# Kernel optimization log

Hardware: AMD Instinct MI355X
Metric: run time of the kernel (lower is better)

The kernel has to match this reference:

```python
import jax, jax.numpy as jnp
import numpy as np

D_VOC, P_VOC, M_VOC = 2048, 1024, 4096
H = 256
T = 32
LD, LP, LM = 24, 12, 20


def _norm_adj(key, n):
    # binary graph + self loops, row-normalized (matches GCN.normalize(adj+I))
    a = (jax.random.uniform(key, (n, n)) < 0.002).astype(jnp.float32)
    a = a + jnp.eye(n, dtype=jnp.float32)
    rs = a.sum(axis=1)
    rinv = jnp.where(rs > 0, 1.0 / rs, 0.0)
    return rinv[:, None] * a


def setup_inputs() -> dict:
    key = jax.random.key(0)
    ks = jax.random.split(key, 32)
    s = float(1.0 / np.sqrt(H))
    u = lambda k, shape, sc: jax.random.uniform(k, shape, minval=-sc, maxval=sc, dtype=jnp.float32)
    inp = {
        'diag_codes': jax.random.randint(ks[0], (T, LD), 0, D_VOC),
        'proc_codes': jax.random.randint(ks[1], (T, LP), 0, P_VOC),
        'med_codes': jax.random.randint(ks[2], (T - 1, LM), 0, M_VOC),
        'diag_emb': u(ks[3], (D_VOC, H), 0.1),
        'proc_emb': u(ks[4], (P_VOC, H), 0.1),
        'gru_d_wih': u(ks[5], (3 * H, H), s), 'gru_d_whh': u(ks[6], (3 * H, H), s),
        'gru_d_bih': u(ks[7], (3 * H,), s), 'gru_d_bhh': u(ks[8], (3 * H,), s),
        'gru_p_wih': u(ks[9], (3 * H, H), s), 'gru_p_whh': u(ks[10], (3 * H, H), s),
        'gru_p_bih': u(ks[11], (3 * H,), s), 'gru_p_bhh': u(ks[12], (3 * H,), s),
        'q_w': u(ks[13], (2 * H, H), s), 'q_b': u(ks[14], (H,), s),
        'adj_ehr': _norm_adj(ks[15], M_VOC),
        'adj_ddi': _norm_adj(ks[16], M_VOC),
        'w1_ehr': u(ks[17], (M_VOC, H), s), 'b1_ehr': u(ks[18], (H,), s),
        'w2_ehr': u(ks[19], (H, H), s), 'b2_ehr': u(ks[20], (H,), s),
        'w1_ddi': u(ks[21], (M_VOC, H), s), 'b1_ddi': u(ks[22], (H,), s),
        'w2_ddi': u(ks[23], (H, H), s), 'b2_ddi': u(ks[24], (H,), s),
        'inter': jax.random.normal(ks[25], (1,), dtype=jnp.float32) / H,
        'proj_w': u(ks[26], (2 * H, H), s), 'proj_b': u(ks[27], (H,), s),
    }
    return inp


def _gru(x, wih, whh, bih, bhh):
    # torch.nn.GRU cell math; x: [T, H] -> outputs [T, H]
    def step(h, xt):
        gi = xt @ wih.T + bih
        gh = h @ whh.T + bhh
        ir, iz, inn = jnp.split(gi, 3)
        hr, hz, hn = jnp.split(gh, 3)
        r = jax.nn.sigmoid(ir + hr)
        z = jax.nn.sigmoid(iz + hz)
        n = jnp.tanh(inn + r * hn)
        h2 = (1.0 - z) * n + z * h
        return h2, h2
    _, ys = jax.lax.scan(step, jnp.zeros((x.shape[-1],), x.dtype), x)
    return ys


def _gcn(adj, w1, b1, w2, b2):
    # input features are identity, so first support mm(I, w1) == w1
    h1 = jax.nn.relu(adj @ w1 + b1)
    return adj @ (h1 @ w2) + b2


def reference(diag_codes, proc_codes, med_codes, diag_emb, proc_emb,
              gru_d_wih, gru_d_whh, gru_d_bih, gru_d_bhh,
              gru_p_wih, gru_p_whh, gru_p_bih, gru_p_bhh,
              q_w, q_b, adj_ehr, adj_ddi,
              w1_ehr, b1_ehr, w2_ehr, b2_ehr,
              w1_ddi, b1_ddi, w2_ddi, b2_ddi,
              inter, proj_w, proj_b):
    # ---- PatientEncoder: gather + sum codes per visit, GRU over visits ----
    seq_d = diag_emb[diag_codes].sum(axis=1)            # [T, H]
    seq_p = proc_emb[proc_codes].sum(axis=1)            # [T, H]
    od = _gru(seq_d, gru_d_wih, gru_d_whh, gru_d_bih, gru_d_bhh)
    op = _gru(seq_p, gru_p_wih, gru_p_whh, gru_p_bih, gru_p_bhh)
    feats = jnp.concatenate([od, op], axis=-1)          # [T, 2H]
    queries = jax.nn.relu(feats) @ q_w + q_b            # [T, H] (Sequential(ReLU, Linear))
    query = queries[-1:]                                # [1, H]
    history_keys = queries[:-1]                         # [T-1, H]
    # multi-hot history medication values (scatter)
    tm1 = med_codes.shape[0]
    history_values = jnp.zeros((tm1, M_VOC), jnp.float32).at[
        jnp.arange(tm1)[:, None], med_codes].set(1.0)   # [T-1, M_VOC]
    # ---- PriorEncoder ----
    prior = _gcn(adj_ehr, w1_ehr, b1_ehr, w2_ehr, b2_ehr) \
        - inter[0] * _gcn(adj_ddi, w1_ddi, b1_ddi, w2_ddi, b2_ddi)  # [M_VOC, H]
    w_emb = jax.nn.softmax(query @ prior.T, axis=-1)    # [1, M_VOC]
    # diag(w) @ prior == broadcast row-scale (the fused gather-weighted-scale)
    gc1 = w_emb.reshape(-1, 1) * prior                  # [M_VOC, H]
    visit_w = jax.nn.softmax(query @ history_keys.T, axis=-1)  # [1, T-1]
    wv = (visit_w @ history_values).reshape(-1, 1)      # [M_VOC, 1]
    gc2 = wv * prior                                    # [M_VOC, H]
    return jnp.concatenate([gc1, gc2], axis=-1) @ proj_w + proj_b  # [M_VOC, H]
```

## Files before the change

kernel.cpp:

```cpp
#include <hip/hip_runtime.h>
#include <hip/hip_bf16.h>

#define HD   256
#define TT   32
#define MV   4096
#define LD_  24
#define LP_  12
#define LM_  20
#define MAXNZ 96

typedef _Float16 h2v __attribute__((ext_vector_type(2)));
typedef _Float16 h8  __attribute__((ext_vector_type(8)));

__device__ __forceinline__ float fdot2(h2v a, h2v b, float c) {
#if __has_builtin(__builtin_amdgcn_fdot2)
  return __builtin_amdgcn_fdot2(a, b, c, false);
#else
  return c + (float)a[0] * (float)b[0] + (float)a[1] * (float)b[1];
#endif
}

#define PIN2(x) { float _t = __builtin_bit_cast(float, x); \
                  asm volatile("" : "+v"(_t));             \
                  x = __builtin_bit_cast(h2v, _t); }

__global__ __launch_bounds__(768) void k01_prep(
    const float* __restrict__ whh_d, const float* __restrict__ whh_p,
    h8* __restrict__ wt,
    const int* __restrict__ dc, const int* __restrict__ pc,
    const float* __restrict__ demb, const float* __restrict__ pemb,
    const float* __restrict__ wih_d, const float* __restrict__ bih_d,
    const float* __restrict__ wih_p, const float* __restrict__ bih_p,
    float* __restrict__ GI)
{
  if (blockIdx.y < 2) {
    const int i = blockIdx.x, b = blockIdx.y, g = threadIdx.x;
    const float* whh = b ? whh_p : whh_d;
    const float* src = whh + (size_t)g * HD + 8 * i;
    h8 v;
#pragma unroll
    for (int e = 0; e < 8; ++e) v[e] = (_Float16)src[e];
    wt[((size_t)b * 32 + i) * 768 + g] = v;
    return;
  }
  const int t = blockIdx.x, b = blockIdx.y - 2;
  const int* codes = b ? pc : dc;
  const int L = b ? LP_ : LD_;
  const float* emb = b ? pemb : demb;
  const float* wih = b ? wih_p : wih_d;
  const float* bih = b ? bih_p : bih_d;
  __shared__ float s[HD];
  const int j = threadIdx.x;
  if (j < HD) {
    float acc = 0.f;
    for (int l = 0; l < L; ++l) acc += emb[(size_t)codes[t * L + l] * HD + j];
    s[j] = acc;
  }
  __syncthreads();
  const int g = j;
  float acc = bih[g];
  const float* wr = wih + (size_t)g * HD;
  for (int k = 0; k < HD; k += 4) {
    float4 w4 = *(const float4*)(wr + k);
    acc = fmaf(w4.x, s[k], acc);
    acc = fmaf(w4.y, s[k + 1], acc);
    acc = fmaf(w4.z, s[k + 2], acc);
    acc = fmaf(w4.w, s[k + 3], acc);
  }
  GI[((size_t)b * TT + t) * 768 + g] = acc;
}

#define LOADROW(EV, ADJROW)                                        \
  _Pragma("unroll")                                                \
  for (int c = 0; c < 16; ++c)                                     \
    EV[c] = *(const float4*)((ADJROW) + c * 256 + lane * 4);

#define PROCESS(EV, RG)                                                 \
  {                                                                     \
    int cl = 0;                                                         \
    _Pragma("unroll")                                                   \
    for (int c = 0; c < 16; ++c)                                        \
      cl += (EV[c].x != 0.f) + (EV[c].y != 0.f) +                       \
            (EV[c].z != 0.f) + (EV[c].w != 0.f);                        \
    int pref = cl;                                                      \
    _Pragma("unroll")                                                   \
    for (int ofs = 1; ofs < 64; ofs <<= 1) {                            \
      int v = __shfl_up(pref, ofs, 64);                                 \
      if (lane >= ofs) pref += v;                                       \
    }                                                                   \
    const int total = __shfl(pref, 63, 64);                             \
    int pos = pref - cl;                                                \
    int* cg = cols_g + (size_t)(RG) * MAXNZ;                            \
    float* vg = vals_g + (size_t)(RG) * MAXNZ;                          \
    _Pragma("unroll")                                                   \
    for (int c = 0; c < 16; ++c) {                                      \
      const float vv[4] = {EV[c].x, EV[c].y, EV[c].z, EV[c].w};         \
      _Pragma("unroll")                                                 \
      for (int e = 0; e < 4; ++e) {                                     \
        if (vv[e] != 0.f) {                                             \
          if (pos < MAXNZ) { cg[pos] = c * 256 + lane * 4 + e;          \
                             vg[pos] = vv[e]; }                         \
          ++pos;                                                        \
        }                                                               \
      }                                                                 \
    }                                                                   \
    if (lane == 0) cnt_g[RG] = total > MAXNZ ? MAXNZ : total;           \
  }

#define ROWPTR(RG) (((RG) >> 12 ? adj_d : adj_e) + (size_t)((RG) & (MV - 1)) * MV)

__global__ __launch_bounds__(512)
__attribute__((amdgpu_waves_per_eu(2, 2)))
void k23_fused(
    const float* __restrict__ GI, const h8* __restrict__ wt,
    const float* __restrict__ bhh_d, const float* __restrict__ bhh_p,
    float* __restrict__ feats,
    const float* __restrict__ adj_e, const float* __restrict__ adj_d,
    int* __restrict__ cnt_g, int* __restrict__ cols_g,
    float* __restrict__ vals_g)
{
  __shared__ h8 hbuf[2][32];

  if (blockIdx.x < 2) {
    const int b = blockIdx.x, t = threadIdx.x;
    const int p = t >> 1;
    const int hk = t & 1;
    const float* gi = GI + (size_t)b * TT * 768;
    const float* bhh = b ? bhh_p : bhh_d;

    h2v w[192];
    {
      const h8* wbase = wt + (size_t)b * 32 * 768;
#pragma unroll
      for (int r3 = 0; r3 < 3; ++r3) {
#pragma unroll
        for (int ii = 0; ii < 16; ++ii) {
          union { h8 v; h2v q[4]; } u;
          u.v = wbase[(size_t)(hk * 16 + ii) * 768 + r3 * 256 + p];
          w[(r3 * 16 + ii) * 4 + 0] = u.q[0];
          w[(r3 * 16 + ii) * 4 + 1] = u.q[1];
          w[(r3 * 16 + ii) * 4 + 2] = u.q[2];
          w[(r3 * 16 + ii) * 4 + 3] = u.q[3];
        }
      }
    }
#pragma unroll
    for (int i = 0; i < 192; ++i) PIN2(w[i])

    const float bh_r = bhh[p], bh_z = bhh[256 + p], bh_n = bhh[512 + p];
    float hreg = 0.f;
    if (t < 256) ((_Float16*)&hbuf[0][0])[t] = (_Float16)0.f;
    __syncthreads();

    for (int tt = 0; tt < TT; ++tt) {
      const float* git = gi + tt * 768;
      float ir = 0.f, iz = 0.f, inn = 0.f;
      if (hk == 0) { ir = git[p]; iz = git[256 + p]; inn = git[512 + p]; }

      const h8* hb = hbuf[tt & 1];
      float dr0 = 0.f, dr1 = 0.f, dz0 = 0.f, dz1 = 0.f, dn0 = 0.f, dn1 = 0.f;
#pragma unroll
      for (int ii = 0; ii < 16; ++ii) {
        union { h8 v; h2v q[4]; } u;
        u.v = hb[hk * 16 + ii];
        dr0 = fdot2(w[(0 * 16 + ii) * 4 + 0], u.q[0], dr0);
        dr1 = fdot2(w[(0 * 16 + ii) * 4 + 1], u.q[1], dr1);
        dr0 = fdot2(w[(0 * 16 + ii) * 4 + 2], u.q[2], dr0);
        dr1 = fdot2(w[(0 * 16 + ii) * 4 + 3], u.q[3], dr1);
        dz0 = fdot2(w[(1 * 16 + ii) * 4 + 0], u.q[0], dz0);
        dz1 = fdot2(w[(1 * 16 + ii) * 4 + 1], u.q[1], dz1);
        dz0 = fdot2(w[(1 * 16 + ii) * 4 + 2], u.q[2], dz0);
        dz1 = fdot2(w[(1 * 16 + ii) * 4 + 3], u.q[3], dz1);
        dn0 = fdot2(w[(2 * 16 + ii) * 4 + 0], u.q[0], dn0);
        dn1 = fdot2(w[(2 * 16 + ii) * 4 + 1], u.q[1], dn1);
        dn0 = fdot2(w[(2 * 16 + ii) * 4 + 2], u.q[2], dn0);
        dn1 = fdot2(w[(2 * 16 + ii) * 4 + 3], u.q[3], dn1);
      }
      float dr = dr0 + dr1, dz = dz0 + dz1, dn = dn0 + dn1;
      dr += __shfl_xor(dr, 1, 64);
      dz += __shfl_xor(dz, 1, 64);
      dn += __shfl_xor(dn, 1, 64);
      if (hk == 0) {
        const float hr = dr + bh_r, hz = dz + bh_z, hn = dn + bh_n;
        const float r = 1.f / (1.f + __expf(-(ir + hr)));
        const float z = 1.f / (1.f + __expf(-(iz + hz)));
        const float n = tanhf(inn + r * hn);
        hreg = (1.f - z) * n + z * hreg;
        ((_Float16*)&hbuf[(tt & 1) ^ 1][0])[p] = (_Float16)hreg;
        feats[(size_t)tt * 512 + b * HD + p] = hreg;
      }
      __syncthreads();
    }
    return;
  }

  const int w = threadIdx.x >> 6, lane = threadIdx.x & 63;
  const int rg0 = (blockIdx.x - 2) * 8 + w;
  const int r0 = rg0, r1 = rg0 + 2032, r2 = rg0 + 4064, r3 = rg0 + 6096,
            r4 = rg0 + 8128;
  const bool has5 = (r4 < 2 * MV);

  float4 evA[16], evB[16];
  LOADROW(evA, ROWPTR(r0))
  LOADROW(evB, ROWPTR(r1))
  PROCESS(evA, r0)
  LOADROW(evA, ROWPTR(r2))
  PROCESS(evB, r1)
  LOADROW(evB, ROWPTR(r3))
  PROCESS(evA, r2)
  if (has5) { LOADROW(evA, ROWPTR(r4)) }
  PROCESS(evB, r3)
  if (has5) { PROCESS(evA, r4) }
}

__global__ __launch_bounds__(256) void k2b_queries(
    const float* __restrict__ feats, const float* __restrict__ q_w,
    const float* __restrict__ q_b, float* __restrict__ queries)
{
  const int t = blockIdx.x, j = threadIdx.x;
  __shared__ float f[512];
  f[j] = fmaxf(feats[(size_t)t * 512 + j], 0.f);
  f[j + 256] = fmaxf(feats[(size_t)t * 512 + 256 + j], 0.f);
  __syncthreads();
  float acc = q_b[j];
  for (int k = 0; k < 512; ++k) acc = fmaf(f[k], q_w[(size_t)k * HD + j], acc);
  queries[(size_t)t * HD + j] = acc;
}

__global__ __launch_bounds__(512) void k45_z(
    const int* __restrict__ cnt_g, const int* __restrict__ cols_g,
    const float* __restrict__ vals_g,
    const float* __restrict__ w1_e, const float* __restrict__ b1_e,
    const float* __restrict__ w1_d, const float* __restrict__ b1_d,
    const float* __restrict__ w2_e, const float* __restrict__ w2_d,
    float* __restrict__ zz)
{
  const int blk = blockIdx.x, b = blockIdx.y;
  const int t = threadIdx.x;
  __shared__ float tile[8][HD];
  __shared__ float part[8][HD];

  {
    const int w = t >> 6, lane = t & 63;
    const int rg = b * MV + blk * 8 + w;
    const float* w1 = b ? w1_d : w1_e;
    const float* b1 = b ? b1_d : b1_e;
    const int n = cnt_g[rg];
    const int* cg = cols_g + (size_t)rg * MAXNZ;
    const float* vg = vals_g + (size_t)rg * MAXNZ;
    float4 acc = *(const float4*)(b1 + lane * 4);
    for (int k = 0; k < n; ++k) {
      const int col = cg[k];
      const float v = vg[k];
      const float4 wv4 = *(const float4*)(w1 + (size_t)col * HD + lane * 4);
      acc.x = fmaf(v, wv4.x, acc.x);
      acc.y = fmaf(v, wv4.y, acc.y);
      acc.z = fmaf(v, wv4.z, acc.z);
      acc.w = fmaf(v, wv4.w, acc.w);
    }
    float4* dst = (float4*)&tile[w][lane * 4];
    dst->x = fmaxf(acc.x, 0.f); dst->y = fmaxf(acc.y, 0.f);
    dst->z = fmaxf(acc.z, 0.f); dst->w = fmaxf(acc.w, 0.f);
  }
  __syncthreads();

  const int j = t & 255, half = t >> 8;
  const float* w2 = b ? w2_d : w2_e;
  float acc[8];
#pragma unroll
  for (int r = 0; r < 8; ++r) acc[r] = 0.f;
  const int k0 = half * 128;
  for (int k = k0; k < k0 + 128; k += 4) {
    float wa = w2[(size_t)(k + 0) * HD + j];
    float wb = w2[(size_t)(k + 1) * HD + j];
    float wc = w2[(size_t)(k + 2) * HD + j];
    float wd = w2[(size_t)(k + 3) * HD + j];
#pragma unroll
    for (int r = 0; r < 8; ++r) {
      float4 tv = *(const float4*)&tile[r][k];
      acc[r] = fmaf(tv.x, wa, acc[r]);
      acc[r] = fmaf(tv.y, wb, acc[r]);
      acc[r] = fmaf(tv.z, wc, acc[r]);
      acc[r] = fmaf(tv.w, wd, acc[r]);
    }
  }
  if (half == 1) {
#pragma unroll
    for (int r = 0; r < 8; ++r) part[r][j] = acc[r];
  }
  __syncthreads();
  if (half == 0) {
    float* zb = zz + (size_t)b * MV * HD + (size_t)blk * 8 * HD;
#pragma unroll
    for (int r = 0; r < 8; ++r) zb[r * HD + j] = acc[r] + part[r][j];
  }
}

__global__ __launch_bounds__(256) void k5_prior(
    const float* __restrict__ zz, const int* __restrict__ cnt_g,
    const int* __restrict__ cols_g, const float* __restrict__ vals_g,
    const float* __restrict__ b2_e, const float* __restrict__ b2_d,
    const float* __restrict__ inter, const float* __restrict__ queries,
    float* __restrict__ prior, float* __restrict__ s1)
{
  const int r = blockIdx.x, j = threadIdx.x;
  __shared__ float red[256];
  float acc_e = b2_e[j];
  {
    const int ne = cnt_g[r];
    const int* ce = cols_g + (size_t)r * MAXNZ;
    const float* ve = vals_g + (size_t)r * MAXNZ;
    for (int k = 0; k < ne; ++k)
      acc_e = fmaf(ve[k], zz[(size_t)ce[k] * HD + j], acc_e);
  }
  float acc_d = b2_d[j];
  {
    const int nd = cnt_g[MV + r];
    const int* cd = cols_g + (size_t)(MV + r) * MAXNZ;
    const float* vd = vals_g + (size_t)(MV + r) * MAXNZ;
    const float* zd = zz + (size_t)MV * HD;
    for (int k = 0; k < nd; ++k)
      acc_d = fmaf(vd[k], zd[(size_t)cd[k] * HD + j], acc_d);
  }
  const float pr = acc_e - inter[0] * acc_d;
  prior[(size_t)r * HD + j] = pr;
  red[j] = queries[31 * HD + j] * pr;
  __syncthreads();
  for (int s = 128; s > 0; s >>= 1) {
    if (j < s) red[j] += red[j + s];
    __syncthreads();
  }
  if (j == 0) s1[r] = red[0];
}

__global__ __launch_bounds__(1024) void k6a_softmax(
    const float* __restrict__ s1, const float* __restrict__ queries,
    float* __restrict__ w_emb, float* __restrict__ visw)
{
  const int j = threadIdx.x;
  __shared__ float red[1024];
  __shared__ float s2[31];
  float m = -1e30f;
  for (int i = j; i < MV; i += 1024) m = fmaxf(m, s1[i]);
  red[j] = m;
  __syncthreads();
  for (int s = 512; s > 0; s >>= 1) {
    if (j < s) red[j] = fmaxf(red[j], red[j + s]);
    __syncthreads();
  }
  const float mx = red[0];
  __syncthreads();
  float sum = 0.f;
  for (int i = j; i < MV; i += 1024) sum += __expf(s1[i] - mx);
  red[j] = sum;
  __syncthreads();
  for (int s = 512; s > 0; s >>= 1) {
    if (j < s) red[j] += red[j + s];
    __syncthreads();
  }
  const float inv = 1.f / red[0];
  for (int i = j; i < MV; i += 1024) w_emb[i] = __expf(s1[i] - mx) * inv;

  if (j < 31) {
    float acc = 0.f;
    for (int k = 0; k < HD; ++k)
      acc = fmaf(queries[31 * HD + k], queries[(size_t)j * HD + k], acc);
    s2[j] = acc;
  }
  __syncthreads();
  if (j == 0) {
    float mm = -1e30f;
    for (int t = 0; t < 31; ++t) mm = fmaxf(mm, s2[t]);
    float ss = 0.f;
    for (int t = 0; t < 31; ++t) ss += __expf(s2[t] - mm);
    const float is = 1.f / ss;
    for (int t = 0; t < 31; ++t) visw[t] = __expf(s2[t] - mm) * is;
  }
}

__global__ __launch_bounds__(1024) void k6b_wv(
    const int* __restrict__ med, const float* __restrict__ visw,
    float* __restrict__ wv)
{
  __shared__ int mc[31 * LM_];
  __shared__ float vw[31];
  const int j = threadIdx.x;
  if (j < 31 * LM_) mc[j] = med[j];
  if (j < 31) vw[j] = visw[j];
  __syncthreads();
  const int m = blockIdx.x * 1024 + j;
  float acc = 0.f;
  for (int t = 0; t < 31; ++t) {
    bool found = false;
#pragma unroll
    for (int l = 0; l < LM_; ++l) found = found || (mc[t * LM_ + l] == m);
    if (found) acc += vw[t];
  }
  wv[m] = acc;
}

__global__ __launch_bounds__(512) void k7_out(
    const float* __restrict__ prior, const float* __restrict__ w_emb,
    const float* __restrict__ wv, const float* __restrict__ proj_w,
    const float* __restrict__ proj_b, float* __restrict__ out)
{
  const int blk = blockIdx.x;
  const int t = threadIdx.x;
  const int j = t & 255, half = t >> 8;
  const int r0 = blk * 8;
  __shared__ float tile[8][HD];
  __shared__ float part[8][HD];
  __shared__ float we[8], wvv[8];
  {
    float4* t4 = (float4*)tile;
    const float4* s4 = (const float4*)(prior + (size_t)r0 * HD);
    t4[t] = s4[t];
  }
  if (t < 8) { we[t] = w_emb[r0 + t]; wvv[t] = wv[r0 + t]; }
  __syncthreads();
  const float* wmat = proj_w + (size_t)half * HD * HD;
  float acc[8];
#pragma unroll
  for (int r = 0; r < 8; ++r) acc[r] = 0.f;
  for (int k = 0; k < HD; k += 4) {
    float wa = wmat[(size_t)(k + 0) * HD + j];
    float wb = wmat[(size_t)(k + 1) * HD + j];
    float wc = wmat[(size_t)(k + 2) * HD + j];
    float wd = wmat[(size_t)(k + 3) * HD + j];
#pragma unroll
    for (int r = 0; r < 8; ++r) {
      float4 tv = *(const float4*)&tile[r][k];
      acc[r] = fmaf(tv.x, wa, acc[r]);
      acc[r] = fmaf(tv.y, wb, acc[r]);
      acc[r] = fmaf(tv.z, wc, acc[r]);
      acc[r] = fmaf(tv.w, wd, acc[r]);
    }
  }
  if (half == 1) {
#pragma unroll
    for (int r = 0; r < 8; ++r) part[r][j] = acc[r];
  }
  __syncthreads();
  if (half == 0) {
    const float pb = proj_b[j];
#pragma unroll
    for (int r = 0; r < 8; ++r)
      out[(size_t)(r0 + r) * HD + j] = we[r] * acc[r] + wvv[r] * part[r][j] + pb;
  }
}

extern "C" void kernel_launch(void* const* d_in, const int* in_sizes, int n_in,
                              void* d_out, int out_size, void* d_ws, size_t ws_size,
                              hipStream_t stream) {
  const int* diag_codes = (const int*)d_in[0];
  const int* proc_codes = (const int*)d_in[1];
  const int* med_codes  = (const int*)d_in[2];
  const float* diag_emb = (const float*)d_in[3];
  const float* proc_emb = (const float*)d_in[4];
  const float* wih_d = (const float*)d_in[5];
  const float* whh_d = (const float*)d_in[6];
  const float* bih_d = (const float*)d_in[7];
  const float* bhh_d = (const float*)d_in[8];
  const float* wih_p = (const float*)d_in[9];
  const float* whh_p = (const float*)d_in[10];
  const float* bih_p = (const float*)d_in[11];
  const float* bhh_p = (const float*)d_in[12];
  const float* q_w = (const float*)d_in[13];
  const float* q_b = (const float*)d_in[14];
  const float* adj_ehr = (const float*)d_in[15];
  const float* adj_ddi = (const float*)d_in[16];
  const float* w1_ehr = (const float*)d_in[17];
  const float* b1_ehr = (const float*)d_in[18];
  const float* w2_ehr = (const float*)d_in[19];
  const float* b2_ehr = (const float*)d_in[20];
  const float* w1_ddi = (const float*)d_in[21];
  const float* b1_ddi = (const float*)d_in[22];
  const float* w2_ddi = (const float*)d_in[23];
  const float* b2_ddi = (const float*)d_in[24];
  const float* inter = (const float*)d_in[25];
  const float* proj_w = (const float*)d_in[26];
  const float* proj_b = (const float*)d_in[27];
  float* out = (float*)d_out;

  float* ws = (float*)d_ws;
  size_t off = 0;
  float* GI      = ws + off; off += 2 * TT * 768;
  float* feats   = ws + off; off += TT * 512;
  float* queries = ws + off; off += TT * HD;
  float* zz      = ws + off; off += 2 * (size_t)MV * HD;
  float* prior   = ws + off; off += (size_t)MV * HD;
  float* s1      = ws + off; off += MV;
  float* w_emb   = ws + off; off += MV;
  float* visw    = ws + off; off += 32;
  float* wv      = ws + off; off += MV;
  int*   cnt_g   = (int*)(ws + off); off += 2 * MV;
  int*   cols_g  = (int*)(ws + off); off += 2 * (size_t)MV * MAXNZ;
  float* vals_g  = ws + off; off += 2 * (size_t)MV * MAXNZ;
  h8*    wt      = (h8*)(ws + off); off += 2 * 32 * 768 * 4;
  (void)ws_size; (void)in_sizes; (void)n_in; (void)out_size;

  k01_prep<<<dim3(32, 4), 768, 0, stream>>>(whh_d, whh_p, wt,
      diag_codes, proc_codes, diag_emb, proc_emb,
      wih_d, bih_d, wih_p, bih_p, GI);
  k23_fused<<<256, 512, 0, stream>>>(GI, wt, bhh_d, bhh_p, feats,
      adj_ehr, adj_ddi, cnt_g, cols_g, vals_g);
  k2b_queries<<<TT, 256, 0, stream>>>(feats, q_w, q_b, queries);
  k45_z<<<dim3(MV / 8, 2), 512, 0, stream>>>(cnt_g, cols_g, vals_g,
      w1_ehr, b1_ehr, w1_ddi, b1_ddi, w2_ehr, w2_ddi, zz);
  k5_prior<<<MV, 256, 0, stream>>>(zz, cnt_g, cols_g, vals_g, b2_ehr, b2_ddi,
      inter, queries, prior, s1);
  k6a_softmax<<<1, 1024, 0, stream>>>(s1, queries, w_emb, visw);
  k6b_wv<<<MV / 1024, 1024, 0, stream>>>(med_codes, visw, wv);
  k7_out<<<MV / 8, 512, 0, stream>>>(prior, w_emb, wv, proj_w, proj_b, out);
}
```

Before: 205.7 us.

## Split fused GRU/adjacency scan kernel and fold wv computation into output kernel

The fused kernel, where two blocks ran the serial GRU while 254 blocks each scanned several adjacency rows, is split into a wide scan kernel with one wave per row (2048 blocks, register-light chunked loads) and a separate two-block GRU kernel launched after it. This serialises the GRU behind the scan instead of overlapping the two, but lets the scan use full occupancy without the GRU's register-heavy launch constraints. The standalone wv kernel is removed and its multi-hot visit-weight lookup is computed inside k7_out with a warp reduction, saving one launch and a global round trip. The risk is losing the overlap of the latency-bound GRU with the bandwidth-bound scan.

```diff
diff --git a/kernel.cpp b/kernel.cpp
--- a/kernel.cpp
+++ b/kernel.cpp
@@ -70,147 +70,148 @@
   GI[((size_t)b * TT + t) * 768 + g] = acc;
 }
 
-#define LOADROW(EV, ADJROW)                                        \
-  _Pragma("unroll")                                                \
-  for (int c = 0; c < 16; ++c)                                     \
-    EV[c] = *(const float4*)((ADJROW) + c * 256 + lane * 4);
-
-#define PROCESS(EV, RG)                                                 \
+__global__ __launch_bounds__(512)
+__attribute__((amdgpu_waves_per_eu(2, 2)))
+void k2_gru(
+    const float* __restrict__ GI, const h8* __restrict__ wt,
+    const float* __restrict__ bhh_d, const float* __restrict__ bhh_p,
+    float* __restrict__ feats)
+{
+  const int b = blockIdx.x, t = threadIdx.x;
+  const int p = t >> 1;
+  const int hk = t & 1;
+  const float* gi = GI + (size_t)b * TT * 768;
+  const float* bhh = b ? bhh_p : bhh_d;
+
+  __shared__ h8 hbuf[2][32];
+
+  h2v w[192];
+  {
+    const h8* wbase = wt + (size_t)b * 32 * 768;
+#pragma unroll
+    for (int r3 = 0; r3 < 3; ++r3) {
+#pragma unroll
+      for (int ii = 0; ii < 16; ++ii) {
+        union { h8 v; h2v q[4]; } u;
+        u.v = wbase[(size_t)(hk * 16 + ii) * 768 + r3 * 256 + p];
+        w[(r3 * 16 + ii) * 4 + 0] = u.q[0];
+        w[(r3 * 16 + ii) * 4 + 1] = u.q[1];
+        w[(r3 * 16 + ii) * 4 + 2] = u.q[2];
+        w[(r3 * 16 + ii) * 4 + 3] = u.q[3];
+      }
+    }
+  }
+#pragma unroll
+  for (int i = 0; i < 192; ++i) PIN2(w[i])
+
+  const float bh_r = bhh[p], bh_z = bhh[256 + p], bh_n = bhh[512 + p];
+  float hreg = 0.f;
+  if (t < 256) ((_Float16*)&hbuf[0][0])[t] = (_Float16)0.f;
+  __syncthreads();
+
+  for (int tt = 0; tt < TT; ++tt) {
+    const float* git = gi + tt * 768;
+    float ir = 0.f, iz = 0.f, inn = 0.f;
+    if (hk == 0) { ir = git[p]; iz = git[256 + p]; inn = git[512 + p]; }
+
+    const h8* hb = hbuf[tt & 1];
+    float dr0 = 0.f, dr1 = 0.f, dz0 = 0.f, dz1 = 0.f, dn0 = 0.f, dn1 = 0.f;
+#pragma unroll
+    for (int ii = 0; ii < 16; ++ii) {
+      union { h8 v; h2v q[4]; } u;
+      u.v = hb[hk * 16 + ii];
+      dr0 = fdot2(w[(0 * 16 + ii) * 4 + 0], u.q[0], dr0);
+      dr1 = fdot2(w[(0 * 16 + ii) * 4 + 1], u.q[1], dr1);
+      dr0 = fdot2(w[(0 * 16 + ii) * 4 + 2], u.q[2], dr0);
+      dr1 = fdot2(w[(0 * 16 + ii) * 4 + 3], u.q[3], dr1);
+      dz0 = fdot2(w[(1 * 16 + ii) * 4 + 0], u.q[0], dz0);
+      dz1 = fdot2(w[(1 * 16 + ii) * 4 + 1], u.q[1], dz1);
+      dz0 = fdot2(w[(1 * 16 + ii) * 4 + 2], u.q[2], dz0);
+      dz1 = fdot2(w[(1 * 16 + ii) * 4 + 3], u.q[3], dz1);
+      dn0 = fdot2(w[(2 * 16 + ii) * 4 + 0], u.q[0], dn0);
+      dn1 = fdot2(w[(2 * 16 + ii) * 4 + 1], u.q[1], dn1);
+      dn0 = fdot2(w[(2 * 16 + ii) * 4 + 2], u.q[2], dn0);
+      dn1 = fdot2(w[(2 * 16 + ii) * 4 + 3], u.q[3], dn1);
+    }
+    float dr = dr0 + dr1, dz = dz0 + dz1, dn = dn0 + dn1;
+    dr += __shfl_xor(dr, 1, 64);
+    dz += __shfl_xor(dz, 1, 64);
+    dn += __shfl_xor(dn, 1, 64);
+    if (hk == 0) {
+      const float hr = dr + bh_r, hz = dz + bh_z, hn = dn + bh_n;
+      const float r = 1.f / (1.f + __expf(-(ir + hr)));
+      const float z = 1.f / (1.f + __expf(-(iz + hz)));
+      const float n = tanhf(inn + r * hn);
+      hreg = (1.f - z) * n + z * hreg;
+      ((_Float16*)&hbuf[(tt & 1) ^ 1][0])[p] = (_Float16)hreg;
+      feats[(size_t)tt * 512 + b * HD + p] = hreg;
+    }
+    __syncthreads();
+  }
+}
+
+#define LOADC(V0, V1, V2, V3, COFF)                               \
+  V0 = *(const float4*)(adj + (COFF) + 0 * 256 + lane * 4);       \
+  V1 = *(const float4*)(adj + (COFF) + 1 * 256 + lane * 4);       \
+  V2 = *(const float4*)(adj + (COFF) + 2 * 256 + lane * 4);       \
+  V3 = *(const float4*)(adj + (COFF) + 3 * 256 + lane * 4);
+
+#define PROCC(V0, V1, V2, V3, COFF)                                     \
   {                                                                     \
     int cl = 0;                                                         \
-    _Pragma("unroll")                                                   \
-    for (int c = 0; c < 16; ++c)                                        \
-      cl += (EV[c].x != 0.f) + (EV[c].y != 0.f) +                       \
-            (EV[c].z != 0.f) + (EV[c].w != 0.f);                        \
+    cl += (V0.x != 0.f) + (V0.y != 0.f) + (V0.z != 0.f) + (V0.w != 0.f);\
+    cl += (V1.x != 0.f) + (V1.y != 0.f) + (V1.z != 0.f) + (V1.w != 0.f);\
+    cl += (V2.x != 0.f) + (V2.y != 0.f) + (V2.z != 0.f) + (V2.w != 0.f);\
+    cl += (V3.x != 0.f) + (V3.y != 0.f) + (V3.z != 0.f) + (V3.w != 0.f);\
     int pref = cl;                                                      \
     _Pragma("unroll")                                                   \
     for (int ofs = 1; ofs < 64; ofs <<= 1) {                            \
       int v = __shfl_up(pref, ofs, 64);                                 \
       if (lane >= ofs) pref += v;                                       \
     }                                                                   \
-    const int total = __shfl(pref, 63, 64);                             \
-    int pos = pref - cl;                                                \
-    int* cg = cols_g + (size_t)(RG) * MAXNZ;                            \
-    float* vg = vals_g + (size_t)(RG) * MAXNZ;                          \
+    const int ctotal = __shfl(pref, 63, 64);                            \
+    int pos = base + pref - cl;                                         \
+    const float4 vv4[4] = {V0, V1, V2, V3};                             \
     _Pragma("unroll")                                                   \
-    for (int c = 0; c < 16; ++c) {                                      \
-      const float vv[4] = {EV[c].x, EV[c].y, EV[c].z, EV[c].w};         \
+    for (int k = 0; k < 4; ++k) {                                       \
+      const float vv[4] = {vv4[k].x, vv4[k].y, vv4[k].z, vv4[k].w};     \
       _Pragma("unroll")                                                 \
       for (int e = 0; e < 4; ++e) {                                     \
         if (vv[e] != 0.f) {                                             \
-          if (pos < MAXNZ) { cg[pos] = c * 256 + lane * 4 + e;          \
+          if (pos < MAXNZ) { cg[pos] = (COFF) + k * 256 + lane * 4 + e; \
                              vg[pos] = vv[e]; }                         \
           ++pos;                                                        \
         }                                                               \
       }                                                                 \
     }                                                                   \
-    if (lane == 0) cnt_g[RG] = total > MAXNZ ? MAXNZ : total;           \
-  }
-
-#define ROWPTR(RG) (((RG) >> 12 ? adj_d : adj_e) + (size_t)((RG) & (MV - 1)) * MV)
-
-__global__ __launch_bounds__(512)
-__attribute__((amdgpu_waves_per_eu(2, 2)))
-void k23_fused(
-    const float* __restrict__ GI, const h8* __restrict__ wt,
-    const float* __restrict__ bhh_d, const float* __restrict__ bhh_p,
-    float* __restrict__ feats,
+    base += ctotal;                                                     \
+  }
+
+__global__ __launch_bounds__(256) void k3_scan(
     const float* __restrict__ adj_e, const float* __restrict__ adj_d,
     int* __restrict__ cnt_g, int* __restrict__ cols_g,
     float* __restrict__ vals_g)
 {
-  __shared__ h8 hbuf[2][32];
-
-  if (blockIdx.x < 2) {
-    const int b = blockIdx.x, t = threadIdx.x;
-    const int p = t >> 1;
-    const int hk = t & 1;
-    const float* gi = GI + (size_t)b * TT * 768;
-    const float* bhh = b ? bhh_p : bhh_d;
-
-    h2v w[192];
-    {
-      const h8* wbase = wt + (size_t)b * 32 * 768;
-#pragma unroll
-      for (int r3 = 0; r3 < 3; ++r3) {
-#pragma unroll
-        for (int ii = 0; ii < 16; ++ii) {
-          union { h8 v; h2v q[4]; } u;
-          u.v = wbase[(size_t)(hk * 16 + ii) * 768 + r3 * 256 + p];
-          w[(r3 * 16 + ii) * 4 + 0] = u.q[0];
-          w[(r3 * 16 + ii) * 4 + 1] = u.q[1];
-          w[(r3 * 16 + ii) * 4 + 2] = u.q[2];
-          w[(r3 * 16 + ii) * 4 + 3] = u.q[3];
-        }
-      }
-    }
-#pragma unroll
-    for (int i = 0; i < 192; ++i) PIN2(w[i])
-
-    const float bh_r = bhh[p], bh_z = bhh[256 + p], bh_n = bhh[512 + p];
-    float hreg = 0.f;
-    if (t < 256) ((_Float16*)&hbuf[0][0])[t] = (_Float16)0.f;
-    __syncthreads();
-
-    for (int tt = 0; tt < TT; ++tt) {
-      const float* git = gi + tt * 768;
-      float ir = 0.f, iz = 0.f, inn = 0.f;
-      if (hk == 0) { ir = git[p]; iz = git[256 + p]; inn = git[512 + p]; }
-
-      const h8* hb = hbuf[tt & 1];
-      float dr0 = 0.f, dr1 = 0.f, dz0 = 0.f, dz1 = 0.f, dn0 = 0.f, dn1 = 0.f;
-#pragma unroll
-      for (int ii = 0; ii < 16; ++ii) {
-        union { h8 v; h2v q[4]; } u;
-        u.v = hb[hk * 16 + ii];
-        dr0 = fdot2(w[(0 * 16 + ii) * 4 + 0], u.q[0], dr0);
-        dr1 = fdot2(w[(0 * 16 + ii) * 4 + 1], u.q[1], dr1);
-        dr0 = fdot2(w[(0 * 16 + ii) * 4 + 2], u.q[2], dr0);
-        dr1 = fdot2(w[(0 * 16 + ii) * 4 + 3], u.q[3], dr1);
-        dz0 = fdot2(w[(1 * 16 + ii) * 4 + 0], u.q[0], dz0);
-        dz1 = fdot2(w[(1 * 16 + ii) * 4 + 1], u.q[1], dz1);
-        dz0 = fdot2(w[(1 * 16 + ii) * 4 + 2], u.q[2], dz0);
-        dz1 = fdot2(w[(1 * 16 + ii) * 4 + 3], u.q[3], dz1);
-        dn0 = fdot2(w[(2 * 16 + ii) * 4 + 0], u.q[0], dn0);
-        dn1 = fdot2(w[(2 * 16 + ii) * 4 + 1], u.q[1], dn1);
-        dn0 = fdot2(w[(2 * 16 + ii) * 4 + 2], u.q[2], dn0);
-        dn1 = fdot2(w[(2 * 16 + ii) * 4 + 3], u.q[3], dn1);
-      }
-      float dr = dr0 + dr1, dz = dz0 + dz1, dn = dn0 + dn1;
-      dr += __shfl_xor(dr, 1, 64);
-      dz += __shfl_xor(dz, 1, 64);
-      dn += __shfl_xor(dn, 1, 64);
-      if (hk == 0) {
-        const float hr = dr + bh_r, hz = dz + bh_z, hn = dn + bh_n;
-        const float r = 1.f / (1.f + __expf(-(ir + hr)));
-        const float z = 1.f / (1.f + __expf(-(iz + hz)));
-        const float n = tanhf(inn + r * hn);
-        hreg = (1.f - z) * n + z * hreg;
-        ((_Float16*)&hbuf[(tt & 1) ^ 1][0])[p] = (_Float16)hreg;
-        feats[(size_t)tt * 512 + b * HD + p] = hreg;
-      }
-      __syncthreads();
-    }
-    return;
-  }
-
   const int w = threadIdx.x >> 6, lane = threadIdx.x & 63;
-  const int rg0 = (blockIdx.x - 2) * 8 + w;
-  const int r0 = rg0, r1 = rg0 + 2032, r2 = rg0 + 4064, r3 = rg0 + 6096,
-            r4 = rg0 + 8128;
-  const bool has5 = (r4 < 2 * MV);
-
-  float4 evA[16], evB[16];
-  LOADROW(evA, ROWPTR(r0))
-  LOADROW(evB, ROWPTR(r1))
-  PROCESS(evA, r0)
-  LOADROW(evA, ROWPTR(r2))
-  PROCESS(evB, r1)
-  LOADROW(evB, ROWPTR(r3))
-  PROCESS(evA, r2)
-  if (has5) { LOADROW(evA, ROWPTR(r4)) }
-  PROCESS(evB, r3)
-  if (has5) { PROCESS(evA, r4) }
+  const int rg = blockIdx.x * 4 + w;
+  const int bsel = rg >> 12;
+  const int r = rg & (MV - 1);
+  const float* adj = (bsel ? adj_d : adj_e) + (size_t)r * MV;
+  int* cg = cols_g + (size_t)rg * MAXNZ;
+  float* vg = vals_g + (size_t)rg * MAXNZ;
+
+  int base = 0;
+  float4 a0, a1, a2, a3, b0, b1, b2, b3;
+  LOADC(a0, a1, a2, a3, 0)
+  LOADC(b0, b1, b2, b3, 1024)
+  PROCC(a0, a1, a2, a3, 0)
+  LOADC(a0, a1, a2, a3, 2048)
+  PROCC(b0, b1, b2, b3, 1024)
+  LOADC(b0, b1, b2, b3, 3072)
+  PROCC(a0, a1, a2, a3, 2048)
+  PROCC(b0, b1, b2, b3, 3072)
+
+  if (lane == 0) cnt_g[rg] = base > MAXNZ ? MAXNZ : base;
 }
 
 __global__ __launch_bounds__(256) void k2b_queries(
@@ -378,31 +379,11 @@
   }
 }
 
-__global__ __launch_bounds__(1024) void k6b_wv(
-    const int* __restrict__ med, const float* __restrict__ visw,
-    float* __restrict__ wv)
-{
-  __shared__ int mc[31 * LM_];
-  __shared__ float vw[31];
-  const int j = threadIdx.x;
-  if (j < 31 * LM_) mc[j] = med[j];
-  if (j < 31) vw[j] = visw[j];
-  __syncthreads();
-  const int m = blockIdx.x * 1024 + j;
-  float acc = 0.f;
-  for (int t = 0; t < 31; ++t) {
-    bool found = false;
-#pragma unroll
-    for (int l = 0; l < LM_; ++l) found = found || (mc[t * LM_ + l] == m);
-    if (found) acc += vw[t];
-  }
-  wv[m] = acc;
-}
-
 __global__ __launch_bounds__(512) void k7_out(
     const float* __restrict__ prior, const float* __restrict__ w_emb,
-    const float* __restrict__ wv, const float* __restrict__ proj_w,
-    const float* __restrict__ proj_b, float* __restrict__ out)
+    const float* __restrict__ visw, const int* __restrict__ med,
+    const float* __restrict__ proj_w, const float* __restrict__ proj_b,
+    float* __restrict__ out)
 {
   const int blk = blockIdx.x;
   const int t = threadIdx.x;
@@ -411,13 +392,31 @@
   __shared__ float tile[8][HD];
   __shared__ float part[8][HD];
   __shared__ float we[8], wvv[8];
+  __shared__ int mc[31 * LM_];
   {
     float4* t4 = (float4*)tile;
     const float4* s4 = (const float4*)(prior + (size_t)r0 * HD);
     t4[t] = s4[t];
   }
-  if (t < 8) { we[t] = w_emb[r0 + t]; wvv[t] = wv[r0 + t]; }
-  __syncthreads();
+  for (int i = t; i < 31 * LM_; i += 512) mc[i] = med[i];
+  if (t < 8) we[t] = w_emb[r0 + t];
+  __syncthreads();
+
+  if (half == 0) {
+    const int r = j >> 5, tp = j & 31;
+    float contrib = 0.f;
+    if (tp < 31) {
+      const int m = r0 + r;
+      bool found = false;
+#pragma unroll
+      for (int l = 0; l < LM_; ++l) found = found || (mc[tp * LM_ + l] == m);
+      if (found) contrib = visw[tp];
+    }
+#pragma unroll
+    for (int msk = 16; msk > 0; msk >>= 1) contrib += __shfl_xor(contrib, msk, 32);
+    if (tp == 0) wvv[r] = contrib;
+  }
+
   const float* wmat = proj_w + (size_t)half * HD * HD;
   float acc[8];
 #pragma unroll
@@ -492,7 +491,6 @@
   float* s1      = ws + off; off += MV;
   float* w_emb   = ws + off; off += MV;
   float* visw    = ws + off; off += 32;
-  float* wv      = ws + off; off += MV;
   int*   cnt_g   = (int*)(ws + off); off += 2 * MV;
   int*   cols_g  = (int*)(ws + off); off += 2 * (size_t)MV * MAXNZ;
   float* vals_g  = ws + off; off += 2 * (size_t)MV * MAXNZ;
@@ -502,14 +500,15 @@
   k01_prep<<<dim3(32, 4), 768, 0, stream>>>(whh_d, whh_p, wt,
       diag_codes, proc_codes, diag_emb, proc_emb,
       wih_d, bih_d, wih_p, bih_p, GI);
-  k23_fused<<<256, 512, 0, stream>>>(GI, wt, bhh_d, bhh_p, feats,
-      adj_ehr, adj_ddi, cnt_g, cols_g, vals_g);
+  k3_scan<<<2 * MV / 4, 256, 0, stream>>>(adj_ehr, adj_ddi,
+      cnt_g, cols_g, vals_g);
+  k2_gru<<<2, 512, 0, stream>>>(GI, wt, bhh_d, bhh_p, feats);
   k2b_queries<<<TT, 256, 0, stream>>>(feats, q_w, q_b, queries);
   k45_z<<<dim3(MV / 8, 2), 512, 0, stream>>>(cnt_g, cols_g, vals_g,
       w1_ehr, b1_ehr, w1_ddi, b1_ddi, w2_ehr, w2_ddi, zz);
   k5_prior<<<MV, 256, 0, stream>>>(zz, cnt_g, cols_g, vals_g, b2_ehr, b2_ddi,
       inter, queries, prior, s1);
   k6a_softmax<<<1, 1024, 0, stream>>>(s1, queries, w_emb, visw);
-  k6b_wv<<<MV / 1024, 1024, 0, stream>>>(med_codes, visw, wv);
-  k7_out<<<MV / 8, 512, 0, stream>>>(prior, w_emb, wv, proj_w, proj_b, out);
-}
+  k7_out<<<MV / 8, 512, 0, stream>>>(prior, w_emb, visw, med_codes,
+      proj_w, proj_b, out);
+}
```

Measured after the change: 208.2 us. No clear change (+1.2%).
